# Kernel optimization log

Hardware: AMD Instinct MI355X
Metric: run time of the kernel (lower is better)

## Reference

```python
import jax, jax.numpy as jnp
import numpy as np

N_NODES = 100000
N_EDGES = 3200000
D_FEAT = 128


def setup_inputs() -> dict:
    key = jax.random.key(0)
    k1, k2, k3, k4 = jax.random.split(key, 4)
    edge_row = jax.random.randint(k1, (N_EDGES,), 0, N_NODES)
    edge_col = jax.random.randint(k2, (N_EDGES,), 0, N_NODES)
    edge_val = jax.random.uniform(k3, (N_EDGES,), dtype=jnp.float32)
    embs = jax.random.normal(k4, (N_NODES, D_FEAT), dtype=jnp.float32)
    return {
        "edge_row": edge_row,
        "edge_col": edge_col,
        "edge_val": edge_val,
        "embs": embs,
        "n_nodes": N_NODES,
    }


def reference(edge_row, edge_col, edge_val, embs, n_nodes):
    # out[r] = sum_{e: row[e]==r} val[e] * embs[col[e]]  == (sparse adj) @ embs
    msgs = embs[edge_col] * edge_val[:, None]  # [E, D] gather + scale
    return jax.ops.segment_sum(msgs, edge_row, num_segments=n_nodes)  # [N, D]
```

## Files before the change

### kernel.cpp

```cpp
#include <hip/hip_runtime.h>
#include <hip/hip_fp16.h>


#define D_FEAT 128
#define CSHIFT 9
#define CROWS 512
#define MAXNBC 256
#define PAD 16
#define BLK1 256
#define EPT1 32
#define EPB1 (BLK1 * EPT1)
#define BLK2 1024

__device__ __forceinline__ int wave_incl_scan(int x, int lane) {
#pragma unroll
    for (int off = 1; off < 64; off <<= 1) {
        int y = __shfl_up(x, off, 64);
        if (lane >= off) x += y;
    }
    return x;
}

__global__ __launch_bounds__(BLK1) void k_part1(const int* __restrict__ row,
                                                const int* __restrict__ col,
                                                const float* __restrict__ val,
                                                int* __restrict__ gcur,
                                                int2* __restrict__ tmp1,
                                                int n_edges, int nbc, int slot) {
    __shared__ int lcnt[MAXNBC], lcur[MAXNBC], lbase[MAXNBC];
    int tid = threadIdx.x;
    for (int j = tid; j < nbc; j += BLK1) { lcnt[j] = 0; lcur[j] = 0; }
    __syncthreads();

    int base = blockIdx.x * EPB1;
    int r[EPT1];
#pragma unroll
    for (int k = 0; k < EPT1; ++k) {
        int e = base + k * BLK1 + tid;
        r[k] = -1;
        if (e < n_edges) {
            r[k] = row[e];
            atomicAdd(&lcnt[r[k] >> CSHIFT], 1);
        }
    }
    __syncthreads();
    for (int j = tid; j < nbc; j += BLK1)
        if (lcnt[j]) lbase[j] = atomicAdd(&gcur[j * PAD], lcnt[j]);
    __syncthreads();
#pragma unroll
    for (int k = 0; k < EPT1; ++k) {
        if (r[k] >= 0) {
            int e = base + k * BLK1 + tid;
            int b = r[k] >> CSHIFT;
            int i = atomicAdd(&lcur[b], 1);
            int pos = lbase[b] + i;
            if (pos < slot)
                tmp1[(size_t)b * slot + pos] =
                    make_int2(((r[k] & (CROWS - 1)) << 17) | col[e],
                              __float_as_int(val[e]));
        }
    }
}

__global__ __launch_bounds__(BLK2) void k_p2conv(const int2* __restrict__ tmp1,
                                                 const int* __restrict__ gcur,
                                                 int2* __restrict__ pcv,
                                                 int* __restrict__ row_start,
                                                 int* __restrict__ row_cnt,
                                                 int n_nodes, int nbc, int slot,
                                                 const float* __restrict__ embs,
                                                 __half* __restrict__ embs16,
                                                 int n_units) {
    int tid = threadIdx.x;
    if ((int)blockIdx.x >= nbc) {
        int i = (blockIdx.x - nbc) * BLK2 + tid;
        if (i >= n_units) return;
        const float4* src = reinterpret_cast<const float4*>(embs) + (size_t)i * 2;
        float4 f0 = src[0];
        float4 f1 = src[1];
        __half2* dst = reinterpret_cast<__half2*>(embs16) + (size_t)i * 4;
        dst[0] = __floats2half2_rn(f0.x, f0.y);
        dst[1] = __floats2half2_rn(f0.z, f0.w);
        dst[2] = __floats2half2_rn(f1.x, f1.y);
        dst[3] = __floats2half2_rn(f1.z, f1.w);
        return;
    }
    __shared__ int rcnt[CROWS], rstart[CROWS], rcur[CROWS];
    __shared__ int wsum[8];
    __shared__ int s[256];
    int b = blockIdx.x;
    int lane = tid & 63, wid = tid >> 6;

    if (tid < 256) {
        int c = (tid < nbc) ? gcur[tid * PAD] : 0;
        s[tid] = (c > slot) ? slot : c;
    }
    __syncthreads();
    for (int off = 1; off < 256; off <<= 1) {
        int u = (tid < 256 && tid >= off) ? s[tid - off] : 0;
        __syncthreads();
        if (tid < 256) s[tid] += u;
        __syncthreads();
    }
    int cnt = gcur[b * PAD]; if (cnt > slot) cnt = slot;
    int pbase = s[b] - cnt;
    const int2* src = tmp1 + (size_t)b * slot;

    for (int j = tid; j < CROWS; j += BLK2) { rcnt[j] = 0; rcur[j] = 0; }
    __syncthreads();
    for (int i = tid; i < cnt; i += BLK2)
        atomicAdd(&rcnt[((unsigned)src[i].x) >> 17], 1);
    __syncthreads();
    int v = (tid < CROWS) ? rcnt[tid] : 0;
    int incl = wave_incl_scan(v, lane);
    if (lane == 63 && wid < 8) wsum[wid] = incl;
    __syncthreads();
    if (tid < 8) {
        int w = wsum[tid];
        int ss = w;
#pragma unroll
        for (int off = 1; off < 8; off <<= 1) {
            int y = __shfl_up(ss, off, 64);
            if (tid >= off) ss += y;
        }
        wsum[tid] = ss - w;
    }
    __syncthreads();
    if (tid < CROWS) rstart[tid] = wsum[wid] + incl - v;
    __syncthreads();
    if (tid < CROWS) {
        int gr = (b << CSHIFT) + tid;
        if (gr < n_nodes) {
            row_start[gr] = pbase + rstart[tid];
            row_cnt[gr]   = v;
        }
    }
    for (int i = tid; i < cnt; i += BLK2) {
        int2 p = src[i];
        int lr = ((unsigned)p.x) >> 17;
        int pos = pbase + rstart[lr] + atomicAdd(&rcur[lr], 1);
        pcv[pos] = make_int2(p.x & 0x1FFFF, p.y);
    }
}

__global__ __launch_bounds__(256) void k_rows_h(const int2* __restrict__ pcv,
                                                const int* __restrict__ row_start,
                                                const int* __restrict__ row_cnt,
                                                const __half2* __restrict__ eb,
                                                float* __restrict__ out, int n_nodes) {
    int gtid = blockIdx.x * blockDim.x + threadIdx.x;
    int r = gtid >> 6;
    int lane = threadIdx.x & 63;
    if (r >= n_nodes) return;

    int start = row_start[r];
    int end   = start + row_cnt[r];

    float2 acc = make_float2(0.f, 0.f);

    int i = start;
    for (; i + 8 <= end; i += 8) {
        int2 p[8];
#pragma unroll
        for (int k = 0; k < 8; ++k) p[k] = pcv[i + k];
        __half2 h[8];
#pragma unroll
        for (int k = 0; k < 8; ++k) h[k] = eb[(size_t)p[k].x * 64 + lane];
#pragma unroll
        for (int k = 0; k < 8; ++k) {
            float v = __int_as_float(p[k].y);
            float2 f = __half22float2(h[k]);
            acc.x += v * f.x;
            acc.y += v * f.y;
        }
    }
    for (; i < end; ++i) {
        int2 p = pcv[i];
        float v = __int_as_float(p.y);
        float2 f = __half22float2(eb[(size_t)p.x * 64 + lane]);
        acc.x += v * f.x;
        acc.y += v * f.y;
    }
    reinterpret_cast<float2*>(out)[(size_t)r * 64 + lane] = acc;
}

__global__ void gcn_scatter_atomic(const int* __restrict__ edge_row,
                                   const int* __restrict__ edge_col,
                                   const float* __restrict__ edge_val,
                                   const float* __restrict__ embs,
                                   float* __restrict__ out, int n_edges) {
    long long tid = (long long)blockIdx.x * blockDim.x + threadIdx.x;
    int sub = (int)(tid & 31);
    long long edge = tid >> 5;
    if (edge >= n_edges) return;
    int r = edge_row[edge];
    int c = edge_col[edge];
    float v = edge_val[edge];
    const float4* src = reinterpret_cast<const float4*>(embs + (size_t)c * D_FEAT);
    float4 m = src[sub];
    float* dst = out + (size_t)r * D_FEAT + (size_t)sub * 4;
    atomicAdd(dst + 0, m.x * v);
    atomicAdd(dst + 1, m.y * v);
    atomicAdd(dst + 2, m.z * v);
    atomicAdd(dst + 3, m.w * v);
}

extern "C" void kernel_launch(void* const* d_in, const int* in_sizes, int n_in,
                              void* d_out, int out_size, void* d_ws, size_t ws_size,
                              hipStream_t stream) {
    const int*   edge_row = (const int*)d_in[0];
    const int*   edge_col = (const int*)d_in[1];
    const float* edge_val = (const float*)d_in[2];
    const float* embs     = (const float*)d_in[3];
    float*       out      = (float*)d_out;

    const int n_edges = in_sizes[0];
    const int n_nodes = out_size / D_FEAT;
    const int nbc = (n_nodes + CROWS - 1) >> CSHIFT;

    const int avg = (n_edges + nbc - 1) / nbc;
    const int slot = (avg + (avg >> 2) + 2048 + 63) & ~63;

    char* ws = (char*)d_ws;
    const size_t off_pcv       = 0;
    const size_t off_row_start = off_pcv + (size_t)n_edges * 8;
    const size_t off_row_cnt   = off_row_start + (size_t)n_nodes * 4;
    const size_t off_gcur      = off_row_cnt + (size_t)n_nodes * 4;
    const size_t off_embs16    = off_gcur + (size_t)MAXNBC * PAD * 4;
    const size_t full_ws       = off_embs16 + (size_t)n_nodes * D_FEAT * 2;

    bool tmp_fits = ((size_t)nbc * slot * 8 <= (size_t)out_size * 4);
    bool packs_ok = (n_nodes <= 131072) && (nbc <= MAXNBC);

    if (ws_size < full_ws || !tmp_fits || !packs_ok) {
        hipMemsetAsync(d_out, 0, (size_t)out_size * sizeof(float), stream);
        long long total = (long long)n_edges * 32;
        int blocks = (int)((total + 255) / 256);
        gcn_scatter_atomic<<<blocks, 256, 0, stream>>>(edge_row, edge_col, edge_val,
                                                       embs, out, n_edges);
        return;
    }

    int2*   pcv       = (int2*)(ws + off_pcv);
    int*    row_start = (int*)(ws + off_row_start);
    int*    row_cnt   = (int*)(ws + off_row_cnt);
    int*    gcur      = (int*)(ws + off_gcur);
    __half* embs16    = (__half*)(ws + off_embs16);
    int2*   tmp1      = (int2*)d_out;

    hipMemsetAsync(gcur, 0, (size_t)MAXNBC * PAD * 4, stream);

    const int nchunks = (n_edges + EPB1 - 1) / EPB1;
    const int n_units = n_nodes * (D_FEAT / 8);
    const int conv_blocks = (n_units + BLK2 - 1) / BLK2;

    k_part1<<<nchunks, BLK1, 0, stream>>>(edge_row, edge_col, edge_val,
                                          gcur, tmp1, n_edges, nbc, slot);
    k_p2conv<<<nbc + conv_blocks, BLK2, 0, stream>>>(
        tmp1, gcur, pcv, row_start, row_cnt, n_nodes, nbc, slot,
        embs, embs16, n_units);

    long long rows_threads = (long long)n_nodes * 64;
    int rblocks = (int)((rows_threads + 255) / 256);
    k_rows_h<<<rblocks, 256, 0, stream>>>(pcv, row_start, row_cnt,
                                          (const __half2*)embs16, out, n_nodes);
}
```

Before: 323.2 us.

## Stage partitioned edges in LDS for coalesced bucket writes; split row kernel

The first partition kernel now loads row, col and val together, builds per-bucket local offsets with a block-wide scan, and stages the packed edges in shared memory sorted by bucket. It then writes them out contiguously, using a binary search over the bucket starts, so global stores to tmp1 are coalesced instead of scattered. Edges per thread drop from 32 to 16 to fit the 8192-entry stage buffer in LDS. The row SpMM kernel is also launched as two half-range launches, which adds launch overhead for no obvious gain.

```diff
diff --git a/kernel.cpp b/kernel.cpp
--- a/kernel.cpp
+++ b/kernel.cpp
@@ -8,7 +8,7 @@
 #define MAXNBC 256
 #define PAD 16
 #define BLK1 256
-#define EPT1 32
+#define EPT1 16
 #define EPB1 (BLK1 * EPT1)
 #define BLK2 1024
 
@@ -27,39 +27,87 @@
                                                 int* __restrict__ gcur,
                                                 int2* __restrict__ tmp1,
                                                 int n_edges, int nbc, int slot) {
-    __shared__ int lcnt[MAXNBC], lcur[MAXNBC], lbase[MAXNBC];
-    int tid = threadIdx.x;
+    __shared__ int2 stage[EPB1];
+    __shared__ int lcnt[MAXNBC], lstart[257], lcur[MAXNBC];
+    __shared__ int lbase[MAXNBC], lroom[MAXNBC];
+    __shared__ int wsum[4];
+    int tid = threadIdx.x, lane = tid & 63, wid = tid >> 6;
     for (int j = tid; j < nbc; j += BLK1) { lcnt[j] = 0; lcur[j] = 0; }
     __syncthreads();
 
     int base = blockIdx.x * EPB1;
-    int r[EPT1];
+    int ne = n_edges - base; if (ne > EPB1) ne = EPB1;
+
+    int r[EPT1], c[EPT1]; float v[EPT1];
 #pragma unroll
     for (int k = 0; k < EPT1; ++k) {
         int e = base + k * BLK1 + tid;
         r[k] = -1;
         if (e < n_edges) {
-            r[k] = row[e];
+            r[k] = row[e]; c[k] = col[e]; v[k] = val[e];
             atomicAdd(&lcnt[r[k] >> CSHIFT], 1);
         }
     }
     __syncthreads();
-    for (int j = tid; j < nbc; j += BLK1)
-        if (lcnt[j]) lbase[j] = atomicAdd(&gcur[j * PAD], lcnt[j]);
+    int cv = (tid < nbc) ? lcnt[tid] : 0;
+    int incl = wave_incl_scan(cv, lane);
+    if (lane == 63) wsum[wid] = incl;
+    __syncthreads();
+    if (tid < 4) {
+        int w = wsum[tid];
+        int ss = w;
+#pragma unroll
+        for (int off = 1; off < 4; off <<= 1) {
+            int y = __shfl_up(ss, off, 64);
+            if (tid >= off) ss += y;
+        }
+        wsum[tid] = ss - w;
+    }
+    __syncthreads();
+    int ex = wsum[wid] + incl - cv;
+    lstart[tid] = (tid < nbc) ? ex : ne;
+    if (tid == BLK1 - 1) lstart[256] = ne;
+    if (tid < nbc && cv) {
+        int res = atomicAdd(&gcur[tid * PAD], cv);
+        lbase[tid] = tid * slot + res;
+        lroom[tid] = slot - res;
+    }
+    __syncthreads();
+    if (tid == 0 && nbc < 256) lstart[nbc] = ne;
     __syncthreads();
 #pragma unroll
     for (int k = 0; k < EPT1; ++k) {
         if (r[k] >= 0) {
-            int e = base + k * BLK1 + tid;
             int b = r[k] >> CSHIFT;
-            int i = atomicAdd(&lcur[b], 1);
-            int pos = lbase[b] + i;
-            if (pos < slot)
-                tmp1[(size_t)b * slot + pos] =
-                    make_int2(((r[k] & (CROWS - 1)) << 17) | col[e],
-                              __float_as_int(val[e]));
-        }
-    }
+            int sl = lstart[b] + atomicAdd(&lcur[b], 1);
+            stage[sl] = make_int2(((r[k] & (CROWS - 1)) << 17) | c[k],
+                                  __float_as_int(v[k]));
+        }
+    }
+    __syncthreads();
+#define P1_SEARCH_STORE(ii)                                                \
+    {                                                                      \
+        int _i = (ii);                                                     \
+        int lo = 0;                                                        \
+        lo += (lstart[lo + 128] <= _i) ? 128 : 0;                          \
+        lo += (lstart[lo + 64]  <= _i) ? 64  : 0;                          \
+        lo += (lstart[lo + 32]  <= _i) ? 32  : 0;                          \
+        lo += (lstart[lo + 16]  <= _i) ? 16  : 0;                          \
+        lo += (lstart[lo + 8]   <= _i) ? 8   : 0;                          \
+        lo += (lstart[lo + 4]   <= _i) ? 4   : 0;                          \
+        lo += (lstart[lo + 2]   <= _i) ? 2   : 0;                          \
+        lo += (lstart[lo + 1]   <= _i) ? 1   : 0;                          \
+        int off = _i - lstart[lo];                                         \
+        if (off < lroom[lo])   \
+            tmp1[lbase[lo] + off] = stage[_i];                             \
+    }
+    if (ne == EPB1) {
+#pragma unroll 4
+        for (int k = 0; k < EPT1; ++k) P1_SEARCH_STORE(k * BLK1 + tid);
+    } else {
+        for (int i = tid; i < ne; i += BLK1) P1_SEARCH_STORE(i);
+    }
+#undef P1_SEARCH_STORE
 }
 
 __global__ __launch_bounds__(BLK2) void k_p2conv(const int2* __restrict__ tmp1,
@@ -147,11 +195,12 @@
                                                 const int* __restrict__ row_start,
                                                 const int* __restrict__ row_cnt,
                                                 const __half2* __restrict__ eb,
-                                                float* __restrict__ out, int n_nodes) {
+                                                float* __restrict__ out,
+                                                int r_begin, int r_end) {
     int gtid = blockIdx.x * blockDim.x + threadIdx.x;
-    int r = gtid >> 6;
+    int r = r_begin + (gtid >> 6);
     int lane = threadIdx.x & 63;
-    if (r >= n_nodes) return;
+    if (r >= r_end) return;
 
     int start = row_start[r];
     int end   = start + row_cnt[r];
@@ -260,8 +309,14 @@
         tmp1, gcur, pcv, row_start, row_cnt, n_nodes, nbc, slot,
         embs, embs16, n_units);
 
-    long long rows_threads = (long long)n_nodes * 64;
-    int rblocks = (int)((rows_threads + 255) / 256);
-    k_rows_h<<<rblocks, 256, 0, stream>>>(pcv, row_start, row_cnt,
-                                          (const __half2*)embs16, out, n_nodes);
-}
+    int half = (n_nodes + 1) / 2;
+    for (int k = 0; k < 2; ++k) {
+        int r0 = k * half;
+        int r1 = r0 + half; if (r1 > n_nodes) r1 = n_nodes;
+        if (r1 <= r0) continue;
+        long long thr = (long long)(r1 - r0) * 64;
+        int blocks = (int)((thr + 255) / 256);
+        k_rows_h<<<blocks, 256, 0, stream>>>(pcv, row_start, row_cnt,
+                                             (const __half2*)embs16, out, r0, r1);
+    }
+}
```

New measurement: 310.2 us. -4.0%, faster.
